# Kernel tuning notes

Hardware: AMD Instinct MI355X
Metric: run time of the kernel (lower is better)

The kernel has to match this reference:

```python
import jax, jax.numpy as jnp
import numpy as np

RATE = 2          # attention_rate from __init__
SOFTMAX_SCALE = 10.0  # standard contextual-attention temperature
EPS = 1e-8


def setup_inputs() -> dict:
    key = jax.random.key(0)
    k1, k2 = jax.random.split(key)
    x = jax.random.normal(k1, (1, 128, 192, 192), dtype=jnp.float32)
    # binary hole mask: 1 = hole (to be filled), 0 = valid background
    mask = (jax.random.uniform(k2, (1, 1, 192, 192)) < 0.25).astype(jnp.float32)
    return {"x": x, "mask": mask}


def reference(x, mask):
    b, c, h, w = x.shape
    r = RATE
    hs, ws = h // r, w // r
    n = hs * ws

    # F.interpolate(..., mode='nearest') downsample == strided slice when divisible
    xs = x[:, :, ::r, ::r]            # [b, c, hs, ws]
    ms = mask[:, :, ::r, ::r]         # [b, 1, hs, ws]

    feat = xs.reshape(b, c, n)        # queries (raw) and keys (normalized)
    keys = feat / (jnp.sqrt(jnp.sum(feat * feat, axis=1, keepdims=True)) + EPS)

    # conv-based correlation == all-pairs inner product with normalized bg patches
    scores = jnp.einsum('bcn,bcm->bnm', feat, keys) * SOFTMAX_SCALE  # [b, n, n]

    valid = (ms.reshape(b, 1, n) == 0.0)  # background key locations
    scores = jnp.where(valid, scores, -1e4)
    attn = jax.nn.softmax(scores, axis=-1)
    attn = attn * valid                   # zero out hole keys exactly

    # extract non-overlapping r x r patches from full-res x: [b, n, c*r*r]
    patches = (x.reshape(b, c, hs, r, ws, r)
                 .transpose(0, 2, 4, 1, 3, 5)
                 .reshape(b, n, c * r * r))

    # transposed-conv reconstruction == weighted sum of patches, folded back
    recon = jnp.einsum('bnm,bmd->bnd', attn, patches)   # [b, n, c*r*r]
    recon_img = (recon.reshape(b, hs, ws, c, r, r)
                      .transpose(0, 3, 1, 4, 2, 5)
                      .reshape(b, c, h, w))

    # composite: keep known pixels, fill holes with attended reconstruction
    return x * (1.0 - mask) + recon_img * mask
```

## Files before the change

kernel.cpp:

```cpp
#include <hip/hip_runtime.h>
#include <hip/hip_bf16.h>

typedef _Float16 f16x8 __attribute__((ext_vector_type(8)));
typedef _Float16 f16x4 __attribute__((ext_vector_type(4)));
typedef float    f32x4 __attribute__((ext_vector_type(4)));

#define HW   36864
#define W_   192
#define NS   9216
#define CCH  128
#define DV   512
#define ROWS 64
#define KV   64
#define NT   144

__global__ __launch_bounds__(256) void prep_vt_kernel(const float* __restrict__ x,
        _Float16* __restrict__ Vt, _Float16* __restrict__ F16)
{
    int m = blockIdx.x * 256 + threadIdx.x;
    int d = blockIdx.y;
    int c = d >> 2, di = (d >> 1) & 1, dj = d & 1;
    int i = m / 96, j = m - i * 96;
    float v = x[c * HW + (2 * i + di) * W_ + (2 * j + dj)];
    _Float16 h = (_Float16)v;
    Vt[(size_t)d * NS + m] = h;
    if ((d & 3) == 0) F16[m * CCH + c] = h;
}

__global__ __launch_bounds__(64) void prep_csv_kernel(const _Float16* __restrict__ F16,
        const float* __restrict__ mask, float* __restrict__ csv)
{
    int m = blockIdx.x;
    int t = threadIdx.x;
    float a = (float)F16[m * CCH + 2 * t];
    float b = (float)F16[m * CCH + 2 * t + 1];
    float ss = a * a + b * b;
    #pragma unroll
    for (int off = 1; off <= 32; off <<= 1)
        ss += __shfl_xor(ss, off);
    if (t == 0) {
        int i = m / 96, j = m - i * 96;
        float ms = mask[(2 * i) * W_ + 2 * j];
        csv[m] = (ms == 0.0f) ? 10.0f / (sqrtf(ss) + 1e-8f) : 0.0f;
    }
}

template<int KT>
__global__ __launch_bounds__(256, 3) void flash_kernel(const _Float16* __restrict__ F16,
        const _Float16* __restrict__ Vt, const float* __restrict__ csv,
        _Float16* __restrict__ po, float* __restrict__ av)
{
    constexpr int SPLT = NT / KT;
    __shared__ __align__(16) _Float16 Kb[2][KV * CCH];
    __shared__ __align__(16) _Float16 Pb[2][ROWS * KV];
    __shared__ __align__(16) float    abuf[2][ROWS];
    __shared__ __align__(16) int      flags[2][4];
    __shared__ __align__(16) float    lbuf[ROWS];

    const int tid  = threadIdx.x;
    const int wv   = tid >> 6;
    const int lane = tid & 63;
    const int g    = lane >> 4, c16 = lane & 15;
    const int flat = blockIdx.x;
    const int sp   = flat % SPLT;
    const int rest = flat / SPLT;
    const int n0   = (rest >> 1) * ROWS;
    const int d0   = (rest & 1) * 256;
    const int t0   = sp * KT;
    const int sw   = c16 & 7;

    auto stageK = [&](int nb, int t) {
        #pragma unroll
        for (int j = 0; j < 4; ++j) {
            const int key  = wv * 16 + j * 4 + g;
            const int csrc = (c16 & 8) | ((c16 & 7) ^ (key & 7));
            __builtin_amdgcn_global_load_lds(
                (const __attribute__((address_space(1))) void*)
                    (F16 + (size_t)(t * KV + key) * CCH + csrc * 8),
                (__attribute__((address_space(3))) void*)
                    (&Kb[nb][(wv * 16 + j * 4) * CCH]),
                16, 0, 0);
        }
    };

    f16x8 q[4];
    #pragma unroll
    for (int kk = 0; kk < 4; ++kk)
        q[kk] = *(const f16x8*)(F16 + (n0 + wv * 16 + c16) * CCH + kk * 32 + g * 8);

    f32x4 o[4][4];
    #pragma unroll
    for (int rf = 0; rf < 4; ++rf)
        #pragma unroll
        for (int df = 0; df < 4; ++df) o[rf][df] = 0.0f;
    float m_run = -1e30f, l_run = 0.0f;

    const _Float16* vbase = Vt + (size_t)(d0 + wv * 64 + c16) * NS + g * 8;

    stageK(0, t0);
    __syncthreads();

    for (int tl = 0; tl < KT; ++tl) {
        const int buf = tl & 1;
        const int m0  = (t0 + tl) * KV;

        f16x8 vreg[8];
        #pragma unroll
        for (int kf = 0; kf < 2; ++kf)
            #pragma unroll
            for (int df = 0; df < 4; ++df)
                vreg[kf * 4 + df] = *(const f16x8*)(vbase + (size_t)(df * 16) * NS
                                                    + m0 + kf * 32);

        f32x4 s[4];
        #pragma unroll
        for (int cf = 0; cf < 4; ++cf) s[cf] = 0.0f;
        #pragma unroll
        for (int cf = 0; cf < 4; ++cf) {
            const _Float16* kr = &Kb[buf][(cf * 16 + c16) * CCH];
            #pragma unroll
            for (int kk = 0; kk < 4; ++kk) {
                const int c  = kk * 4 + g;
                const int cc = (c & 8) | ((c & 7) ^ sw);
                s[cf] = __builtin_amdgcn_mfma_f32_16x16x32_f16(
                            *(const f16x8*)(kr + cc * 8), q[kk], s[cf], 0, 0, 0);
            }
        }

        f32x4 cs[4];
        #pragma unroll
        for (int cf = 0; cf < 4; ++cf)
            cs[cf] = *(const f32x4*)(csv + m0 + cf * 16 + g * 4);

        float tm = -1e30f;
        #pragma unroll
        for (int cf = 0; cf < 4; ++cf)
            #pragma unroll
            for (int r = 0; r < 4; ++r)
                tm = fmaxf(tm, (cs[cf][r] > 0.0f) ? s[cf][r] * cs[cf][r] : -1e30f);
        tm = fmaxf(tm, __shfl_xor(tm, 16));
        tm = fmaxf(tm, __shfl_xor(tm, 32));

        float al = 1.0f;
        const bool trig = __any(tm > m_run + 8.0f);
        if (trig) {
            float nm = fmaxf(m_run, tm);
            al = __expf(m_run - nm);
            l_run *= al; m_run = nm;
        }
        if (lane == 0) flags[buf][wv] = trig ? 1 : 0;
        if (g == 0)    abuf[buf][wv * 16 + c16] = al;

        float ps = 0.0f;
        const int prow = wv * 16 + c16;
        #pragma unroll
        for (int cf = 0; cf < 4; ++cf) {
            f16x4 ph;
            #pragma unroll
            for (int r = 0; r < 4; ++r) {
                float e = (cs[cf][r] > 0.0f) ? __expf(s[cf][r] * cs[cf][r] - m_run) : 0.0f;
                ps += e;
                ph[r] = (_Float16)e;
            }
            const int ch = (cf * 2 + (g >> 1)) ^ sw;
            *(f16x4*)(&Pb[buf][prow * KV + ch * 8 + (g & 1) * 4]) = ph;
        }
        ps += __shfl_xor(ps, 16);
        ps += __shfl_xor(ps, 32);
        l_run += ps;

        if (tl + 1 < KT) stageK(buf ^ 1, t0 + tl + 1);

        __syncthreads();

        {
            const int4 fl = *(const int4*)(&flags[buf][0]);
            if (fl.x | fl.y | fl.z | fl.w) {
                #pragma unroll
                for (int rf = 0; rf < 4; ++rf) {
                    f32x4 a4 = *(const f32x4*)(&abuf[buf][rf * 16 + g * 4]);
                    #pragma unroll
                    for (int df = 0; df < 4; ++df)
                        #pragma unroll
                        for (int r = 0; r < 4; ++r) o[rf][df][r] *= a4[r];
                }
            }
        }
        #pragma unroll
        for (int kf = 0; kf < 2; ++kf) {
            f16x8 pa[4];
            #pragma unroll
            for (int rf = 0; rf < 4; ++rf)
                pa[rf] = *(const f16x8*)(&Pb[buf][(rf * 16 + c16) * KV
                                                  + (((kf * 4 + g) ^ sw) * 8)]);
            #pragma unroll
            for (int df = 0; df < 4; ++df)
                #pragma unroll
                for (int rf = 0; rf < 4; ++rf)
                    o[rf][df] = __builtin_amdgcn_mfma_f32_16x16x32_f16(
                                    pa[rf], vreg[kf * 4 + df], o[rf][df], 0, 0, 0);
        }
    }

    if (g == 0) {
        lbuf[wv * 16 + c16] = (l_run > 0.0f) ? 1.0f / l_run : 0.0f;
        if (d0 == 0)
            av[sp * NS + n0 + wv * 16 + c16] =
                (l_run > 0.0f) ? m_run + __logf(l_run) : -1e30f;
    }
    __syncthreads();
    #pragma unroll
    for (int rf = 0; rf < 4; ++rf) {
        f32x4 li = *(const f32x4*)(&lbuf[rf * 16 + g * 4]);
        #pragma unroll
        for (int df = 0; df < 4; ++df) {
            f16x4 res;
            #pragma unroll
            for (int r = 0; r < 4; ++r) res[r] = (_Float16)(o[rf][df][r] * li[r]);
            *(f16x4*)(po + ((size_t)sp * DV + d0 + wv * 64 + df * 16 + c16) * NS
                          + n0 + rf * 16 + g * 4) = res;
        }
    }
}

template<int S>
__global__ __launch_bounds__(192) void combine_kernel(const float* __restrict__ x,
        const float* __restrict__ mask, const _Float16* __restrict__ po,
        const float* __restrict__ av, float* __restrict__ out)
{
    int i = blockIdx.x;
    int c = blockIdx.y;
    int w = threadIdx.x;
    int n = i * 96 + (w >> 1);

    float A = -1e30f;
    #pragma unroll
    for (int s = 0; s < S; ++s) A = fmaxf(A, av[s * NS + n]);
    float wt[S], wsum = 0.0f;
    #pragma unroll
    for (int s = 0; s < S; ++s) {
        float a = av[s * NS + n];
        float e = (a > -1e29f) ? __expf(a - A) : 0.0f;
        wt[s] = e; wsum += e;
    }
    float invw = (wsum > 0.0f) ? 1.0f / wsum : 0.0f;

    #pragma unroll
    for (int di = 0; di < 2; ++di) {
        int h = 2 * i + di;
        int d = c * 4 + di * 2 + (w & 1);
        float rv = 0.0f;
        #pragma unroll
        for (int s = 0; s < S; ++s)
            rv += wt[s] * (float)po[((size_t)s * DV + d) * NS + n];
        rv *= invw;
        float xv = x[c * HW + h * W_ + w];
        float mv = mask[h * W_ + w];
        out[c * HW + h * W_ + w] = xv * (1.0f - mv) + rv * mv;
    }
}

extern "C" void kernel_launch(void* const* d_in, const int* in_sizes, int n_in,
                              void* d_out, int out_size, void* d_ws, size_t ws_size,
                              hipStream_t stream) {
    const float* x    = (const float*)d_in[0];
    const float* mask = (const float*)d_in[1];
    float* out = (float*)d_out;

    char* ws = (char*)d_ws;
    _Float16* Vt  = (_Float16*)(ws);
    _Float16* F16 = (_Float16*)(ws + 9437184);
    float*    csv = (float*)   (ws + 11796480);
    float*    av  = (float*)   (ws + 11833344);
    _Float16* po  = (_Float16*)(ws + 12128256);

    prep_vt_kernel <<<dim3(36, 512), 256, 0, stream>>>(x, Vt, F16);
    prep_csv_kernel<<<NS, 64, 0, stream>>>(F16, mask, csv);

    const size_t base = 12128256ull;
    if (ws_size >= base + 8ull * 9437184ull) {
        flash_kernel<18><<<288 * 8, 256, 0, stream>>>(F16, Vt, csv, po, av);
        combine_kernel<8><<<dim3(96, 128), 192, 0, stream>>>(x, mask, po, av, out);
    } else {
        flash_kernel<36><<<288 * 4, 256, 0, stream>>>(F16, Vt, csv, po, av);
        combine_kernel<4><<<dim3(96, 128), 192, 0, stream>>>(x, mask, po, av, out);
    }
}
```

Baseline: 341.7 us.

## Use exp2-domain softmax, register-staged K prefetch, and MFMA priority boosts

Folds log2(e) into the per-key scale so the online softmax uses exp2 directly, and pre-masks scores so the exp loop drops its branch. Replaces the direct global-to-LDS K staging with a register prefetch issued early in the iteration and written to LDS after the softmax. Wraps both MFMA blocks in s_setprio to favour matrix issue across waves. The register prefetch raises VGPR pressure, which may hurt occupancy under launch_bounds(256,3).

Result: slower. 544.1 us (+59.2%).

```diff
diff --git a/kernel.cpp b/kernel.cpp
--- a/kernel.cpp
+++ b/kernel.cpp
@@ -13,6 +13,10 @@
 #define ROWS 64
 #define KV   64
 #define NT   144
+#define LOG2E 1.44269504089f
+#define LN2   0.69314718056f
+#define THR2  11.5417f
+#define EXP2(x) __builtin_exp2f(x)
 
 __global__ __launch_bounds__(256) void prep_vt_kernel(const float* __restrict__ x,
         _Float16* __restrict__ Vt, _Float16* __restrict__ F16)
@@ -41,7 +45,7 @@
     if (t == 0) {
         int i = m / 96, j = m - i * 96;
         float ms = mask[(2 * i) * W_ + 2 * j];
-        csv[m] = (ms == 0.0f) ? 10.0f / (sqrtf(ss) + 1e-8f) : 0.0f;
+        csv[m] = (ms == 0.0f) ? 10.0f * LOG2E / (sqrtf(ss) + 1e-8f) : 0.0f;
     }
 }
 
@@ -69,17 +73,20 @@
     const int t0   = sp * KT;
     const int sw   = c16 & 7;
 
-    auto stageK = [&](int nb, int t) {
+    f16x8 kpre[4];
+    auto loadK = [&](int t) {
         #pragma unroll
         for (int j = 0; j < 4; ++j) {
-            const int key  = wv * 16 + j * 4 + g;
-            const int csrc = (c16 & 8) | ((c16 & 7) ^ (key & 7));
-            __builtin_amdgcn_global_load_lds(
-                (const __attribute__((address_space(1))) void*)
-                    (F16 + (size_t)(t * KV + key) * CCH + csrc * 8),
-                (__attribute__((address_space(3))) void*)
-                    (&Kb[nb][(wv * 16 + j * 4) * CCH]),
-                16, 0, 0);
+            const int key = wv * 16 + j * 4 + g;
+            kpre[j] = *(const f16x8*)(F16 + (size_t)(t * KV + key) * CCH + c16 * 8);
+        }
+    };
+    auto writeK = [&](int nb) {
+        #pragma unroll
+        for (int j = 0; j < 4; ++j) {
+            const int key = wv * 16 + j * 4 + g;
+            const int ch  = (c16 & 8) | ((c16 & 7) ^ (key & 7));
+            *(f16x8*)(&Kb[nb][key * CCH + ch * 8]) = kpre[j];
         }
     };
 
@@ -93,11 +100,12 @@
     for (int rf = 0; rf < 4; ++rf)
         #pragma unroll
         for (int df = 0; df < 4; ++df) o[rf][df] = 0.0f;
-    float m_run = -1e30f, l_run = 0.0f;
+    float m_run = -20000.0f, l_run = 0.0f;
 
     const _Float16* vbase = Vt + (size_t)(d0 + wv * 64 + c16) * NS + g * 8;
 
-    stageK(0, t0);
+    loadK(t0);
+    writeK(0);
     __syncthreads();
 
     for (int tl = 0; tl < KT; ++tl) {
@@ -112,9 +120,12 @@
                 vreg[kf * 4 + df] = *(const f16x8*)(vbase + (size_t)(df * 16) * NS
                                                     + m0 + kf * 32);
 
+        if (tl + 1 < KT) loadK(t0 + tl + 1);
+
         f32x4 s[4];
         #pragma unroll
         for (int cf = 0; cf < 4; ++cf) s[cf] = 0.0f;
+        __builtin_amdgcn_s_setprio(1);
         #pragma unroll
         for (int cf = 0; cf < 4; ++cf) {
             const _Float16* kr = &Kb[buf][(cf * 16 + c16) * CCH];
@@ -126,6 +137,7 @@
                             *(const f16x8*)(kr + cc * 8), q[kk], s[cf], 0, 0, 0);
             }
         }
+        __builtin_amdgcn_s_setprio(0);
 
         f32x4 cs[4];
         #pragma unroll
@@ -136,16 +148,19 @@
         #pragma unroll
         for (int cf = 0; cf < 4; ++cf)
             #pragma unroll
-            for (int r = 0; r < 4; ++r)
-                tm = fmaxf(tm, (cs[cf][r] > 0.0f) ? s[cf][r] * cs[cf][r] : -1e30f);
+            for (int r = 0; r < 4; ++r) {
+                float v = (cs[cf][r] > 0.0f) ? s[cf][r] * cs[cf][r] : -60000.0f;
+                s[cf][r] = v;
+                tm = fmaxf(tm, v);
+            }
         tm = fmaxf(tm, __shfl_xor(tm, 16));
         tm = fmaxf(tm, __shfl_xor(tm, 32));
 
         float al = 1.0f;
-        const bool trig = __any(tm > m_run + 8.0f);
+        const bool trig = __any(tm > m_run + THR2);
         if (trig) {
             float nm = fmaxf(m_run, tm);
-            al = __expf(m_run - nm);
+            al = EXP2(m_run - nm);
             l_run *= al; m_run = nm;
         }
         if (lane == 0) flags[buf][wv] = trig ? 1 : 0;
@@ -155,13 +170,12 @@
         const int prow = wv * 16 + c16;
         #pragma unroll
         for (int cf = 0; cf < 4; ++cf) {
-            f16x4 ph;
-            #pragma unroll
-            for (int r = 0; r < 4; ++r) {
-                float e = (cs[cf][r] > 0.0f) ? __expf(s[cf][r] * cs[cf][r] - m_run) : 0.0f;
-                ps += e;
-                ph[r] = (_Float16)e;
-            }
+            float e0 = EXP2(s[cf][0] - m_run);
+            float e1 = EXP2(s[cf][1] - m_run);
+            float e2 = EXP2(s[cf][2] - m_run);
+            float e3 = EXP2(s[cf][3] - m_run);
+            ps += (e0 + e1) + (e2 + e3);
+            f16x4 ph = { (_Float16)e0, (_Float16)e1, (_Float16)e2, (_Float16)e3 };
             const int ch = (cf * 2 + (g >> 1)) ^ sw;
             *(f16x4*)(&Pb[buf][prow * KV + ch * 8 + (g & 1) * 4]) = ph;
         }
@@ -169,7 +183,7 @@
         ps += __shfl_xor(ps, 32);
         l_run += ps;
 
-        if (tl + 1 < KT) stageK(buf ^ 1, t0 + tl + 1);
+        if (tl + 1 < KT) writeK(buf ^ 1);
 
         __syncthreads();
 
@@ -186,6 +200,7 @@
                 }
             }
         }
+        __builtin_amdgcn_s_setprio(1);
         #pragma unroll
         for (int kf = 0; kf < 2; ++kf) {
             f16x8 pa[4];
@@ -200,13 +215,14 @@
                     o[rf][df] = __builtin_amdgcn_mfma_f32_16x16x32_f16(
                                     pa[rf], vreg[kf * 4 + df], o[rf][df], 0, 0, 0);
         }
+        __builtin_amdgcn_s_setprio(0);
     }
 
     if (g == 0) {
         lbuf[wv * 16 + c16] = (l_run > 0.0f) ? 1.0f / l_run : 0.0f;
         if (d0 == 0)
             av[sp * NS + n0 + wv * 16 + c16] =
-                (l_run > 0.0f) ? m_run + __logf(l_run) : -1e30f;
+                (l_run > 0.0f) ? m_run * LN2 + __logf(l_run) : -1e30f;
     }
     __syncthreads();
     #pragma unroll
```
